# Optimization experiments

Hardware: AMD Instinct MI355X
Metric: run time of the kernel (lower is better)

The kernel has to match this reference:

```python
import jax, jax.numpy as jnp
import numpy as np

GRID_RES = 32      # sparse_grid_dim
GRID_DIM = 8       # dense cells per sparse block side
NUM_EMB = 12000    # number of sparse blocks
EMB_DIM = 1
N_POINTS = 2000000
N_CELLS = GRID_RES * GRID_DIM  # 256^3 virtual dense grid over [-1,1]^3


def _interp_point(pos, embeddings, block_table):
    """Trilinear interp of a sparse block-grid at one world point in [-1,1]^3.

    embeddings: [NUM_EMB, GRID_DIM^3, EMB_DIM]
    block_table: [GRID_RES]^3 int32, block index or -1 if unallocated.
    Returns (emb [EMB_DIM], valid_all bool).
    """
    xc = (pos + 1.0) * 0.5 * (N_CELLS - 1)            # world -> cell coords
    base = jnp.clip(jnp.floor(xc), 0.0, N_CELLS - 2).astype(jnp.int32)
    frac = xc - base.astype(xc.dtype)
    emb = jnp.zeros((EMB_DIM,), xc.dtype)
    valid_all = jnp.bool_(True)
    for dx in (0, 1):
        for dy in (0, 1):
            for dz in (0, 1):
                corner = base + jnp.array([dx, dy, dz], jnp.int32)
                blk = corner // GRID_DIM                 # sparse block coord
                loc = corner % GRID_DIM                  # local cell coord
                bidx = block_table[blk[0], blk[1], blk[2]]
                valid = bidx >= 0
                li = (loc[0] * GRID_DIM + loc[1]) * GRID_DIM + loc[2]
                e = embeddings[jnp.maximum(bidx, 0), li]
                wx = frac[0] if dx else 1.0 - frac[0]
                wy = frac[1] if dy else 1.0 - frac[1]
                wz = frac[2] if dz else 1.0 - frac[2]
                emb = emb + jnp.where(valid, wx * wy * wz, 0.0) * e
                valid_all = jnp.logical_and(valid_all, valid)
    return emb, valid_all


def setup_inputs() -> dict:
    key = jax.random.key(0)
    k1, k2 = jax.random.split(key, 2)
    positions = jax.random.uniform(k1, (N_POINTS, 3), minval=-1.0, maxval=1.0,
                                   dtype=jnp.float32)
    # original init zeros the embeddings; use small randn for a non-trivial test
    embeddings = 0.1 * jax.random.normal(k2, (NUM_EMB, GRID_DIM ** 3, EMB_DIM),
                                         dtype=jnp.float32)
    # sparse occupancy: NUM_EMB random blocks of the GRID_RES^3 lattice allocated
    rng = np.random.default_rng(0)
    table = -np.ones(GRID_RES ** 3, np.int32)
    table[rng.permutation(GRID_RES ** 3)[:NUM_EMB]] = np.arange(NUM_EMB, dtype=np.int32)
    block_table = jnp.asarray(table.reshape(GRID_RES, GRID_RES, GRID_RES))
    return {"positions": positions, "embeddings": embeddings,
            "block_table": block_table}


@jax.jit
def reference(positions, embeddings, block_table):
    def f(pos):
        e, v = _interp_point(pos, embeddings, block_table)
        return e[0], v
    # value_and_grad mirrors torch.autograd.grad(embedding[...,0], positions)
    (emb, mask), grad_x = jax.vmap(jax.value_and_grad(f, has_aux=True))(positions)
    return emb[:, None], grad_x, mask
```

## Files before the change

### kernel.cpp

```cpp
#include <hip/hip_runtime.h>
#include <hip/hip_bf16.h>

#define GRID_RES 32
#define GRID_DIM 8
#define N_CELLS  256
#define EMB_VOL  512
#define NPT      4
#define BLOCK    512
#define TAB_N    (GRID_RES * GRID_RES * GRID_RES)

__global__ __launch_bounds__(BLOCK) void neural_poisson_interp(
    const float* __restrict__ positions,
    const float* __restrict__ embeddings,
    const int*   __restrict__ block_table,
    float* __restrict__ out,
    int n)
{
    __shared__ short stab[TAB_N];

    {
        const int4* t4 = reinterpret_cast<const int4*>(block_table);
        for (int k = threadIdx.x; k < TAB_N / 4; k += BLOCK) {
            int4 v = t4[k];
            short4 s;
            s.x = (short)v.x; s.y = (short)v.y; s.z = (short)v.z; s.w = (short)v.w;
            *reinterpret_cast<short4*>(&stab[4 * k]) = s;
        }
    }
    __syncthreads();

    int t  = blockIdx.x * blockDim.x + threadIdx.x;
    int i0 = t * NPT;
    if (i0 >= n) return;
    bool full = (i0 + NPT <= n);

    float px[NPT], py[NPT], pz[NPT];
    if (full) {
        const float4* p4 = reinterpret_cast<const float4*>(positions + 3 * (size_t)i0);
        float4 A = p4[0], B = p4[1], C = p4[2];
        px[0] = A.x; py[0] = A.y; pz[0] = A.z;
        px[1] = A.w; py[1] = B.x; pz[1] = B.y;
        px[2] = B.z; py[2] = B.w; pz[2] = C.x;
        px[3] = C.y; py[3] = C.z; pz[3] = C.w;
    } else {
#pragma unroll
        for (int p = 0; p < NPT; ++p) {
            int ip = min(i0 + p, n - 1);
            px[p] = positions[3 * ip + 0];
            py[p] = positions[3 * ip + 1];
            pz[p] = positions[3 * ip + 2];
        }
    }

    float wA[NPT][3], wB[NPT][3];
    int   bidx[NPT][8];
    int   li  [NPT][8];

#pragma unroll
    for (int p = 0; p < NPT; ++p) {
        float xc[3];
        xc[0] = (px[p] + 1.0f) * 0.5f * (float)(N_CELLS - 1);
        xc[1] = (py[p] + 1.0f) * 0.5f * (float)(N_CELLS - 1);
        xc[2] = (pz[p] + 1.0f) * 0.5f * (float)(N_CELLS - 1);

        int base[3];
#pragma unroll
        for (int a = 0; a < 3; ++a) {
            float bf = fminf(fmaxf(floorf(xc[a]), 0.0f), (float)(N_CELLS - 2));
            float fr = xc[a] - bf;
            wA[p][a] = 1.0f - fr;
            wB[p][a] = fr;
            base[a] = (int)bf;
        }

#pragma unroll
        for (int c = 0; c < 8; ++c) {
            int dx = (c >> 2) & 1, dy = (c >> 1) & 1, dz = c & 1;
            int cx = base[0] + dx, cy = base[1] + dy, cz = base[2] + dz;
            bidx[p][c] = stab[((cx >> 3) * GRID_RES + (cy >> 3)) * GRID_RES
                              + (cz >> 3)];
            li[p][c] = ((cx & 7) * GRID_DIM + (cy & 7)) * GRID_DIM + (cz & 7);
        }
    }

    float e[NPT][8];
#pragma unroll
    for (int p = 0; p < NPT; ++p)
#pragma unroll
        for (int c = 0; c < 8; ++c) {
            int b = bidx[p][c] > 0 ? bidx[p][c] : 0;
            e[p][c] = embeddings[b * EMB_VOL + li[p][c]];
        }

    const float scale = 0.5f * (float)(N_CELLS - 1);
    float acc[NPT], gxv[NPT], gyv[NPT], gzv[NPT], mk[NPT];

#pragma unroll
    for (int p = 0; p < NPT; ++p) {
        float a = 0.0f, gx = 0.0f, gy = 0.0f, gz = 0.0f;
        bool vall = true;
#pragma unroll
        for (int c = 0; c < 8; ++c) {
            int dx = (c >> 2) & 1, dy = (c >> 1) & 1, dz = c & 1;
            bool valid = bidx[p][c] >= 0;
            vall = vall && valid;
            float ev = valid ? e[p][c] : 0.0f;
            float wx = dx ? wB[p][0] : wA[p][0];
            float wy = dy ? wB[p][1] : wA[p][1];
            float wz = dz ? wB[p][2] : wA[p][2];
            a  += wx * wy * wz * ev;
            float tgx = wy * wz * ev;
            float tgy = wx * wz * ev;
            float tgz = wx * wy * ev;
            gx += dx ? tgx : -tgx;
            gy += dy ? tgy : -tgy;
            gz += dz ? tgz : -tgz;
        }
        acc[p] = a;
        gxv[p] = scale * gx;
        gyv[p] = scale * gy;
        gzv[p] = scale * gz;
        mk[p]  = vall ? 1.0f : 0.0f;
    }

    float* out_emb  = out;
    float* out_grad = out + (size_t)n;
    float* out_mask = out + 4 * (size_t)n;

    if (full) {
        *reinterpret_cast<float4*>(out_emb + i0) =
            make_float4(acc[0], acc[1], acc[2], acc[3]);
        float4* g4 = reinterpret_cast<float4*>(out_grad + 3 * (size_t)i0);
        g4[0] = make_float4(gxv[0], gyv[0], gzv[0], gxv[1]);
        g4[1] = make_float4(gyv[1], gzv[1], gxv[2], gyv[2]);
        g4[2] = make_float4(gzv[2], gxv[3], gyv[3], gzv[3]);
        *reinterpret_cast<float4*>(out_mask + i0) =
            make_float4(mk[0], mk[1], mk[2], mk[3]);
    } else {
#pragma unroll
        for (int p = 0; p < NPT; ++p) {
            int ip = i0 + p;
            if (ip < n) {
                out_emb[ip]          = acc[p];
                out_grad[3 * ip + 0] = gxv[p];
                out_grad[3 * ip + 1] = gyv[p];
                out_grad[3 * ip + 2] = gzv[p];
                out_mask[ip]         = mk[p];
            }
        }
    }
}

extern "C" void kernel_launch(void* const* d_in, const int* in_sizes, int n_in,
                              void* d_out, int out_size, void* d_ws, size_t ws_size,
                              hipStream_t stream) {
    const float* positions   = (const float*)d_in[0];
    const float* embeddings  = (const float*)d_in[1];
    const int*   block_table = (const int*)d_in[2];

    int n = in_sizes[0] / 3;
    int nthreads = (n + NPT - 1) / NPT;

    float* out = (float*)d_out;

    int grid = (nthreads + BLOCK - 1) / BLOCK;
    neural_poisson_interp<<<grid, BLOCK, 0, stream>>>(
        positions, embeddings, block_table, out, n);
}
```

Baseline: 130.2 us.

## Pre-pack z-adjacent embedding pairs as bf16 and use persistent grid

Adds a pre-pass kernel that builds, for each allocated block, a workspace array of packed bf16 pairs (value at z and z+1, including the neighbour block's first z slice). The main kernel then fetches both z corners with one 32-bit load, halving the embedding gathers per point. It also switches to a grid-stride persistent launch capped at 512 blocks, so the shared-memory table load is amortised over many points. The trade-off is bf16 precision loss on embeddings, an extra launch and a pre-pass over all 32768 table entries, and a slow fallback load when only the z+1 block is allocated.

New measurement: 136.8 us. +5.0%, slower.

```diff
diff --git a/kernel.cpp b/kernel.cpp
--- a/kernel.cpp
+++ b/kernel.cpp
@@ -5,19 +5,216 @@
 #define GRID_DIM 8
 #define N_CELLS  256
 #define EMB_VOL  512
+#define TAB_N    (GRID_RES * GRID_RES * GRID_RES)
 #define NPT      4
 #define BLOCK    512
-#define TAB_N    (GRID_RES * GRID_RES * GRID_RES)
+
+
+__device__ __forceinline__ unsigned bf16rne(float f) {
+    unsigned u = __float_as_uint(f);
+    return (u + 0x7fffu + ((u >> 16) & 1u)) >> 16;
+}
+
+__global__ __launch_bounds__(256) void build_pairs(
+    const float* __restrict__ emb, const int* __restrict__ table,
+    unsigned* __restrict__ pb)
+{
+    int tid = blockIdx.x * 256 + threadIdx.x;
+    int entry = tid >> 6;
+    if (entry >= TAB_N) return;
+    int row = tid & 63;
+    int b = table[entry];
+    if (b < 0) return;
+    int BZ = entry & (GRID_RES - 1);
+    int zn = (BZ < GRID_RES - 1) ? table[entry + 1] : -1;
+
+    const float* src = emb + (size_t)b * EMB_VOL + row * 8;
+    float4 a0 = *reinterpret_cast<const float4*>(src);
+    float4 a1 = *reinterpret_cast<const float4*>(src + 4);
+    float e0=a0.x, e1=a0.y, e2=a0.z, e3=a0.w;
+    float e4=a1.x, e5=a1.y, e6=a1.z, e7=a1.w;
+    float e8 = (zn >= 0) ? emb[(size_t)zn * EMB_VOL + row * 8] : 0.0f;
+
+    unsigned o0 = bf16rne(e0) | (bf16rne(e1) << 16);
+    unsigned o1 = bf16rne(e2) | (bf16rne(e3) << 16);
+    unsigned o2 = bf16rne(e4) | (bf16rne(e5) << 16);
+    unsigned o3 = bf16rne(e6) | (bf16rne(e7) << 16);
+    unsigned o4 = bf16rne(e1) | (bf16rne(e2) << 16);
+    unsigned o5 = bf16rne(e3) | (bf16rne(e4) << 16);
+    unsigned o6 = bf16rne(e5) | (bf16rne(e6) << 16);
+    unsigned o7 = bf16rne(e7) | (bf16rne(e8) << 16);
+
+    uint4* dst = reinterpret_cast<uint4*>(pb + (size_t)b * EMB_VOL + row * 8);
+    dst[0] = make_uint4(o0, o1, o2, o3);
+    dst[1] = make_uint4(o4, o5, o6, o7);
+}
+
+__global__ __launch_bounds__(BLOCK) void interp_pairs(
+    const float* __restrict__ positions,
+    const float* __restrict__ emb,
+    const int*   __restrict__ table,
+    const unsigned* __restrict__ pb,
+    float* __restrict__ out, int n)
+{
+    __shared__ short stab[TAB_N];
+    {
+        const int4* t4 = reinterpret_cast<const int4*>(table);
+        for (int k = threadIdx.x; k < TAB_N / 4; k += BLOCK) {
+            int4 v = t4[k];
+            short4 s;
+            s.x = (short)v.x; s.y = (short)v.y; s.z = (short)v.z; s.w = (short)v.w;
+            *reinterpret_cast<short4*>(&stab[4 * k]) = s;
+        }
+    }
+    __syncthreads();
+
+    int nq = (n + NPT - 1) / NPT;
+    int stride = gridDim.x * BLOCK;
+    for (int q = blockIdx.x * BLOCK + threadIdx.x; q < nq; q += stride) {
+        int i0 = q * NPT;
+        bool full = (i0 + NPT <= n);
+
+        float px[NPT], py[NPT], pz[NPT];
+        if (full) {
+            const float4* p4 = reinterpret_cast<const float4*>(positions + 3 * (size_t)i0);
+            float4 A = p4[0], B = p4[1], C = p4[2];
+            px[0]=A.x; py[0]=A.y; pz[0]=A.z;
+            px[1]=A.w; py[1]=B.x; pz[1]=B.y;
+            px[2]=B.z; py[2]=B.w; pz[2]=C.x;
+            px[3]=C.y; py[3]=C.z; pz[3]=C.w;
+        } else {
+#pragma unroll
+            for (int p = 0; p < NPT; ++p) {
+                int ip = min(i0 + p, n - 1);
+                px[p] = positions[3 * ip + 0];
+                py[p] = positions[3 * ip + 1];
+                pz[p] = positions[3 * ip + 2];
+            }
+        }
+
+        float wA[NPT][3], wB[NPT][3];
+        int tb[NPT][4], tb1[NPT][4];
+        unsigned lx4[NPT];
+        int lzv[NPT];
+        unsigned uu[NPT][4];
+
+#pragma unroll
+        for (int p = 0; p < NPT; ++p) {
+            float xc[3];
+            xc[0] = (px[p] + 1.0f) * 0.5f * (float)(N_CELLS - 1);
+            xc[1] = (py[p] + 1.0f) * 0.5f * (float)(N_CELLS - 1);
+            xc[2] = (pz[p] + 1.0f) * 0.5f * (float)(N_CELLS - 1);
+            int base[3];
+#pragma unroll
+            for (int a = 0; a < 3; ++a) {
+                float bf = fminf(fmaxf(floorf(xc[a]), 0.0f), (float)(N_CELLS - 2));
+                float fr = xc[a] - bf;
+                wA[p][a] = 1.0f - fr;
+                wB[p][a] = fr;
+                base[a] = (int)bf;
+            }
+            int bx = base[0], by = base[1], bz = base[2];
+            lzv[p] = bz & 7;
+            int bzs0 = bz >> 3, bzs1 = (bz + 1) >> 3;
+            unsigned pk = 0;
+#pragma unroll
+            for (int c = 0; c < 4; ++c) {
+                int dx = c >> 1, dy = c & 1;
+                int cx = bx + dx, cy = by + dy;
+                int tbase = ((cx >> 3) * GRID_RES + (cy >> 3)) * GRID_RES;
+                tb [p][c] = stab[tbase + bzs0];
+                tb1[p][c] = stab[tbase + bzs1];
+                unsigned lxly = (unsigned)((cx & 7) * 8 + (cy & 7));
+                pk |= lxly << (8 * c);
+            }
+            lx4[p] = pk;
+        }
+
+#pragma unroll
+        for (int p = 0; p < NPT; ++p) {
+            int lz = lzv[p];
+            int zoff = (lz & 1) ? 4 + (lz >> 1) : (lz >> 1);
+#pragma unroll
+            for (int c = 0; c < 4; ++c) {
+                int b = tb[p][c] > 0 ? tb[p][c] : 0;
+                int lxly = (lx4[p] >> (8 * c)) & 0xff;
+                uu[p][c] = pb[(size_t)b * EMB_VOL + lxly * 8 + zoff];
+            }
+        }
+
+        const float scale = 0.5f * (float)(N_CELLS - 1);
+        float acc[NPT], gxv[NPT], gyv[NPT], gzv[NPT], mk[NPT];
+
+#pragma unroll
+        for (int p = 0; p < NPT; ++p) {
+            float wz0 = wA[p][2], wz1 = wB[p][2];
+            float a = 0.0f, gx = 0.0f, gy = 0.0f, gz = 0.0f;
+            bool vall = true;
+#pragma unroll
+            for (int c = 0; c < 4; ++c) {
+                int dx = c >> 1, dy = c & 1;
+                bool v0 = tb [p][c] >= 0;
+                bool v1 = tb1[p][c] >= 0;
+                vall = vall && v0 && v1;
+                unsigned u = uu[p][c];
+                float e0 = v0 ? __uint_as_float(u << 16) : 0.0f;
+                float e1 = v0 ? __uint_as_float(u & 0xffff0000u) : 0.0f;
+                if (!v0 && v1) {
+                    int lxly = (lx4[p] >> (8 * c)) & 0xff;
+                    e1 = emb[(size_t)tb1[p][c] * EMB_VOL + lxly * 8];
+                }
+                float s = wz0 * e0 + wz1 * e1;
+                float wx = dx ? wB[p][0] : wA[p][0];
+                float wy = dy ? wB[p][1] : wA[p][1];
+                float wxy = wx * wy;
+                a  += wxy * s;
+                gx += dx ? wy * s : -wy * s;
+                gy += dy ? wx * s : -wx * s;
+                gz += wxy * (e1 - e0);
+            }
+            acc[p] = a;
+            gxv[p] = scale * gx;
+            gyv[p] = scale * gy;
+            gzv[p] = scale * gz;
+            mk[p]  = vall ? 1.0f : 0.0f;
+        }
+
+        float* out_emb  = out;
+        float* out_grad = out + (size_t)n;
+        float* out_mask = out + 4 * (size_t)n;
+
+        if (full) {
+            *reinterpret_cast<float4*>(out_emb + i0) =
+                make_float4(acc[0], acc[1], acc[2], acc[3]);
+            float4* g4 = reinterpret_cast<float4*>(out_grad + 3 * (size_t)i0);
+            g4[0] = make_float4(gxv[0], gyv[0], gzv[0], gxv[1]);
+            g4[1] = make_float4(gyv[1], gzv[1], gxv[2], gyv[2]);
+            g4[2] = make_float4(gzv[2], gxv[3], gyv[3], gzv[3]);
+            *reinterpret_cast<float4*>(out_mask + i0) =
+                make_float4(mk[0], mk[1], mk[2], mk[3]);
+        } else {
+#pragma unroll
+            for (int p = 0; p < NPT; ++p) {
+                int ip = i0 + p;
+                if (ip < n) {
+                    out_emb[ip]          = acc[p];
+                    out_grad[3 * ip + 0] = gxv[p];
+                    out_grad[3 * ip + 1] = gyv[p];
+                    out_grad[3 * ip + 2] = gzv[p];
+                    out_mask[ip]         = mk[p];
+                }
+            }
+        }
+    }
+}
 
 __global__ __launch_bounds__(BLOCK) void neural_poisson_interp(
     const float* __restrict__ positions,
     const float* __restrict__ embeddings,
     const int*   __restrict__ block_table,
-    float* __restrict__ out,
-    int n)
+    float* __restrict__ out, int n)
 {
     __shared__ short stab[TAB_N];
-
     {
         const int4* t4 = reinterpret_cast<const int4*>(block_table);
         for (int k = threadIdx.x; k < TAB_N / 4; k += BLOCK) {
@@ -29,7 +226,7 @@
     }
     __syncthreads();
 
-    int t  = blockIdx.x * blockDim.x + threadIdx.x;
+    int t = blockIdx.x * blockDim.x + threadIdx.x;
     int i0 = t * NPT;
     if (i0 >= n) return;
     bool full = (i0 + NPT <= n);
@@ -38,10 +235,10 @@
     if (full) {
         const float4* p4 = reinterpret_cast<const float4*>(positions + 3 * (size_t)i0);
         float4 A = p4[0], B = p4[1], C = p4[2];
-        px[0] = A.x; py[0] = A.y; pz[0] = A.z;
-        px[1] = A.w; py[1] = B.x; pz[1] = B.y;
-        px[2] = B.z; py[2] = B.w; pz[2] = C.x;
-        px[3] = C.y; py[3] = C.z; pz[3] = C.w;
+        px[0]=A.x; py[0]=A.y; pz[0]=A.z;
+        px[1]=A.w; py[1]=B.x; pz[1]=B.y;
+        px[2]=B.z; py[2]=B.w; pz[2]=C.x;
+        px[3]=C.y; py[3]=C.z; pz[3]=C.w;
     } else {
 #pragma unroll
         for (int p = 0; p < NPT; ++p) {
@@ -53,36 +250,31 @@
     }
 
     float wA[NPT][3], wB[NPT][3];
-    int   bidx[NPT][8];
-    int   li  [NPT][8];
-
+    int bidx[NPT][8];
+    int li[NPT][8];
 #pragma unroll
     for (int p = 0; p < NPT; ++p) {
         float xc[3];
-        xc[0] = (px[p] + 1.0f) * 0.5f * (float)(N_CELLS - 1);
-        xc[1] = (py[p] + 1.0f) * 0.5f * (float)(N_CELLS - 1);
-        xc[2] = (pz[p] + 1.0f) * 0.5f * (float)(N_CELLS - 1);
-
+        xc[0] = (px[p] + 1.0f) * 0.5f * 255.0f;
+        xc[1] = (py[p] + 1.0f) * 0.5f * 255.0f;
+        xc[2] = (pz[p] + 1.0f) * 0.5f * 255.0f;
         int base[3];
 #pragma unroll
         for (int a = 0; a < 3; ++a) {
-            float bf = fminf(fmaxf(floorf(xc[a]), 0.0f), (float)(N_CELLS - 2));
+            float bf = fminf(fmaxf(floorf(xc[a]), 0.0f), 254.0f);
             float fr = xc[a] - bf;
             wA[p][a] = 1.0f - fr;
             wB[p][a] = fr;
             base[a] = (int)bf;
         }
-
 #pragma unroll
         for (int c = 0; c < 8; ++c) {
             int dx = (c >> 2) & 1, dy = (c >> 1) & 1, dz = c & 1;
             int cx = base[0] + dx, cy = base[1] + dy, cz = base[2] + dz;
-            bidx[p][c] = stab[((cx >> 3) * GRID_RES + (cy >> 3)) * GRID_RES
-                              + (cz >> 3)];
+            bidx[p][c] = stab[((cx >> 3) * GRID_RES + (cy >> 3)) * GRID_RES + (cz >> 3)];
             li[p][c] = ((cx & 7) * GRID_DIM + (cy & 7)) * GRID_DIM + (cz & 7);
         }
     }
-
     float e[NPT][8];
 #pragma unroll
     for (int p = 0; p < NPT; ++p)
@@ -91,10 +283,8 @@
             int b = bidx[p][c] > 0 ? bidx[p][c] : 0;
             e[p][c] = embeddings[b * EMB_VOL + li[p][c]];
         }
-
-    const float scale = 0.5f * (float)(N_CELLS - 1);
+    const float scale = 127.5f;
     float acc[NPT], gxv[NPT], gyv[NPT], gzv[NPT], mk[NPT];
-
 #pragma unroll
     for (int p = 0; p < NPT; ++p) {
         float a = 0.0f, gx = 0.0f, gy = 0.0f, gz = 0.0f;
@@ -108,7 +298,7 @@
             float wx = dx ? wB[p][0] : wA[p][0];
             float wy = dy ? wB[p][1] : wA[p][1];
             float wz = dz ? wB[p][2] : wA[p][2];
-            a  += wx * wy * wz * ev;
+            a += wx * wy * wz * ev;
             float tgx = wy * wz * ev;
             float tgy = wx * wz * ev;
             float tgz = wx * wy * ev;
@@ -116,17 +306,12 @@
             gy += dy ? tgy : -tgy;
             gz += dz ? tgz : -tgz;
         }
-        acc[p] = a;
-        gxv[p] = scale * gx;
-        gyv[p] = scale * gy;
-        gzv[p] = scale * gz;
-        mk[p]  = vall ? 1.0f : 0.0f;
-    }
-
+        acc[p] = a; gxv[p] = scale * gx; gyv[p] = scale * gy; gzv[p] = scale * gz;
+        mk[p] = vall ? 1.0f : 0.0f;
+    }
     float* out_emb  = out;
     float* out_grad = out + (size_t)n;
     float* out_mask = out + 4 * (size_t)n;
-
     if (full) {
         *reinterpret_cast<float4*>(out_emb + i0) =
             make_float4(acc[0], acc[1], acc[2], acc[3]);
@@ -141,11 +326,11 @@
         for (int p = 0; p < NPT; ++p) {
             int ip = i0 + p;
             if (ip < n) {
-                out_emb[ip]          = acc[p];
+                out_emb[ip] = acc[p];
                 out_grad[3 * ip + 0] = gxv[p];
                 out_grad[3 * ip + 1] = gyv[p];
                 out_grad[3 * ip + 2] = gzv[p];
-                out_mask[ip]         = mk[p];
+                out_mask[ip] = mk[p];
             }
         }
     }
@@ -159,11 +344,24 @@
     const int*   block_table = (const int*)d_in[2];
 
     int n = in_sizes[0] / 3;
-    int nthreads = (n + NPT - 1) / NPT;
-
+    int nblocks = in_sizes[1] / EMB_VOL;
+    size_t pair_bytes = (size_t)nblocks * EMB_VOL * sizeof(unsigned);
     float* out = (float*)d_out;
 
-    int grid = (nthreads + BLOCK - 1) / BLOCK;
-    neural_poisson_interp<<<grid, BLOCK, 0, stream>>>(
-        positions, embeddings, block_table, out, n);
-}
+    if (ws_size >= pair_bytes) {
+        unsigned* pb = (unsigned*)d_ws;
+        build_pairs<<<(TAB_N * 64 + 255) / 256, 256, 0, stream>>>(
+            embeddings, block_table, pb);
+        int nq = (n + NPT - 1) / NPT;
+        int grid = 512;
+        int maxg = (nq + BLOCK - 1) / BLOCK;
+        if (grid > maxg) grid = maxg;
+        interp_pairs<<<grid, BLOCK, 0, stream>>>(
+            positions, embeddings, block_table, pb, out, n);
+    } else {
+        int nthreads = (n + NPT - 1) / NPT;
+        int grid = (nthreads + BLOCK - 1) / BLOCK;
+        neural_poisson_interp<<<grid, BLOCK, 0, stream>>>(
+            positions, embeddings, block_table, out, n);
+    }
+}
```

## Use persistent grid-stride blocks to amortize shared block-table load

Applied to the files above, without the earlier changes.

Switches to a fixed grid of 512 blocks of 1024 threads that grid-stride over point pairs, with two points per iteration instead of four. Each block now loads and converts the block table into shared memory once, so the per-block table load is spread over many more points. The narrower per-thread work may lower memory-level parallelism per thread, and the launch-bounds hint may constrain registers.

Result: slower. 176.7 us (+35.7%).

```diff
diff --git a/kernel.cpp b/kernel.cpp
--- a/kernel.cpp
+++ b/kernel.cpp
@@ -5,11 +5,11 @@
 #define GRID_DIM 8
 #define N_CELLS  256
 #define EMB_VOL  512
-#define NPT      4
-#define BLOCK    512
 #define TAB_N    (GRID_RES * GRID_RES * GRID_RES)
+#define NPT      2
+#define BLOCK    1024
 
-__global__ __launch_bounds__(BLOCK) void neural_poisson_interp(
+__global__ __launch_bounds__(BLOCK, 8) void neural_poisson_interp(
     const float* __restrict__ positions,
     const float* __restrict__ embeddings,
     const int*   __restrict__ block_table,
@@ -17,7 +17,6 @@
     int n)
 {
     __shared__ short stab[TAB_N];
-
     {
         const int4* t4 = reinterpret_cast<const int4*>(block_table);
         for (int k = threadIdx.x; k < TAB_N / 4; k += BLOCK) {
@@ -29,123 +28,119 @@
     }
     __syncthreads();
 
-    int t  = blockIdx.x * blockDim.x + threadIdx.x;
-    int i0 = t * NPT;
-    if (i0 >= n) return;
-    bool full = (i0 + NPT <= n);
-
-    float px[NPT], py[NPT], pz[NPT];
-    if (full) {
-        const float4* p4 = reinterpret_cast<const float4*>(positions + 3 * (size_t)i0);
-        float4 A = p4[0], B = p4[1], C = p4[2];
-        px[0] = A.x; py[0] = A.y; pz[0] = A.z;
-        px[1] = A.w; py[1] = B.x; pz[1] = B.y;
-        px[2] = B.z; py[2] = B.w; pz[2] = C.x;
-        px[3] = C.y; py[3] = C.z; pz[3] = C.w;
-    } else {
-#pragma unroll
-        for (int p = 0; p < NPT; ++p) {
-            int ip = min(i0 + p, n - 1);
-            px[p] = positions[3 * ip + 0];
-            py[p] = positions[3 * ip + 1];
-            pz[p] = positions[3 * ip + 2];
-        }
-    }
-
-    float wA[NPT][3], wB[NPT][3];
-    int   bidx[NPT][8];
-    int   li  [NPT][8];
-
-#pragma unroll
-    for (int p = 0; p < NPT; ++p) {
-        float xc[3];
-        xc[0] = (px[p] + 1.0f) * 0.5f * (float)(N_CELLS - 1);
-        xc[1] = (py[p] + 1.0f) * 0.5f * (float)(N_CELLS - 1);
-        xc[2] = (pz[p] + 1.0f) * 0.5f * (float)(N_CELLS - 1);
-
-        int base[3];
-#pragma unroll
-        for (int a = 0; a < 3; ++a) {
-            float bf = fminf(fmaxf(floorf(xc[a]), 0.0f), (float)(N_CELLS - 2));
-            float fr = xc[a] - bf;
-            wA[p][a] = 1.0f - fr;
-            wB[p][a] = fr;
-            base[a] = (int)bf;
-        }
-
-#pragma unroll
-        for (int c = 0; c < 8; ++c) {
-            int dx = (c >> 2) & 1, dy = (c >> 1) & 1, dz = c & 1;
-            int cx = base[0] + dx, cy = base[1] + dy, cz = base[2] + dz;
-            bidx[p][c] = stab[((cx >> 3) * GRID_RES + (cy >> 3)) * GRID_RES
-                              + (cz >> 3)];
-            li[p][c] = ((cx & 7) * GRID_DIM + (cy & 7)) * GRID_DIM + (cz & 7);
-        }
-    }
-
-    float e[NPT][8];
-#pragma unroll
-    for (int p = 0; p < NPT; ++p)
-#pragma unroll
-        for (int c = 0; c < 8; ++c) {
-            int b = bidx[p][c] > 0 ? bidx[p][c] : 0;
-            e[p][c] = embeddings[b * EMB_VOL + li[p][c]];
-        }
-
-    const float scale = 0.5f * (float)(N_CELLS - 1);
-    float acc[NPT], gxv[NPT], gyv[NPT], gzv[NPT], mk[NPT];
-
-#pragma unroll
-    for (int p = 0; p < NPT; ++p) {
-        float a = 0.0f, gx = 0.0f, gy = 0.0f, gz = 0.0f;
-        bool vall = true;
-#pragma unroll
-        for (int c = 0; c < 8; ++c) {
-            int dx = (c >> 2) & 1, dy = (c >> 1) & 1, dz = c & 1;
-            bool valid = bidx[p][c] >= 0;
-            vall = vall && valid;
-            float ev = valid ? e[p][c] : 0.0f;
-            float wx = dx ? wB[p][0] : wA[p][0];
-            float wy = dy ? wB[p][1] : wA[p][1];
-            float wz = dz ? wB[p][2] : wA[p][2];
-            a  += wx * wy * wz * ev;
-            float tgx = wy * wz * ev;
-            float tgy = wx * wz * ev;
-            float tgz = wx * wy * ev;
-            gx += dx ? tgx : -tgx;
-            gy += dy ? tgy : -tgy;
-            gz += dz ? tgz : -tgz;
-        }
-        acc[p] = a;
-        gxv[p] = scale * gx;
-        gyv[p] = scale * gy;
-        gzv[p] = scale * gz;
-        mk[p]  = vall ? 1.0f : 0.0f;
-    }
-
     float* out_emb  = out;
     float* out_grad = out + (size_t)n;
     float* out_mask = out + 4 * (size_t)n;
 
-    if (full) {
-        *reinterpret_cast<float4*>(out_emb + i0) =
-            make_float4(acc[0], acc[1], acc[2], acc[3]);
-        float4* g4 = reinterpret_cast<float4*>(out_grad + 3 * (size_t)i0);
-        g4[0] = make_float4(gxv[0], gyv[0], gzv[0], gxv[1]);
-        g4[1] = make_float4(gyv[1], gzv[1], gxv[2], gyv[2]);
-        g4[2] = make_float4(gzv[2], gxv[3], gyv[3], gzv[3]);
-        *reinterpret_cast<float4*>(out_mask + i0) =
-            make_float4(mk[0], mk[1], mk[2], mk[3]);
-    } else {
+    int nq = (n + NPT - 1) / NPT;
+    int stride = gridDim.x * BLOCK;
+    for (int q = blockIdx.x * BLOCK + threadIdx.x; q < nq; q += stride) {
+        int i0 = q * NPT;
+        bool full = (i0 + NPT <= n);
+
+        float px[NPT], py[NPT], pz[NPT];
+        if (full) {
+            const float2* p2 = reinterpret_cast<const float2*>(positions + 3 * (size_t)i0);
+            float2 A = p2[0], B = p2[1], C = p2[2];
+            px[0] = A.x; py[0] = A.y; pz[0] = B.x;
+            px[1] = B.y; py[1] = C.x; pz[1] = C.y;
+        } else {
+#pragma unroll
+            for (int p = 0; p < NPT; ++p) {
+                int ip = min(i0 + p, n - 1);
+                px[p] = positions[3 * ip + 0];
+                py[p] = positions[3 * ip + 1];
+                pz[p] = positions[3 * ip + 2];
+            }
+        }
+
+        float wA[NPT][3], wB[NPT][3];
+        int bidx[NPT][8];
+        int li  [NPT][8];
+
 #pragma unroll
         for (int p = 0; p < NPT; ++p) {
-            int ip = i0 + p;
-            if (ip < n) {
-                out_emb[ip]          = acc[p];
-                out_grad[3 * ip + 0] = gxv[p];
-                out_grad[3 * ip + 1] = gyv[p];
-                out_grad[3 * ip + 2] = gzv[p];
-                out_mask[ip]         = mk[p];
+            float xc[3];
+            xc[0] = (px[p] + 1.0f) * 0.5f * (float)(N_CELLS - 1);
+            xc[1] = (py[p] + 1.0f) * 0.5f * (float)(N_CELLS - 1);
+            xc[2] = (pz[p] + 1.0f) * 0.5f * (float)(N_CELLS - 1);
+            int base[3];
+#pragma unroll
+            for (int a = 0; a < 3; ++a) {
+                float bf = fminf(fmaxf(floorf(xc[a]), 0.0f), (float)(N_CELLS - 2));
+                float fr = xc[a] - bf;
+                wA[p][a] = 1.0f - fr;
+                wB[p][a] = fr;
+                base[a] = (int)bf;
+            }
+#pragma unroll
+            for (int c = 0; c < 8; ++c) {
+                int dx = (c >> 2) & 1, dy = (c >> 1) & 1, dz = c & 1;
+                int cx = base[0] + dx, cy = base[1] + dy, cz = base[2] + dz;
+                bidx[p][c] = stab[((cx >> 3) * GRID_RES + (cy >> 3)) * GRID_RES
+                                  + (cz >> 3)];
+                li[p][c] = ((cx & 7) * GRID_DIM + (cy & 7)) * GRID_DIM + (cz & 7);
+            }
+        }
+
+        float e[NPT][8];
+#pragma unroll
+        for (int p = 0; p < NPT; ++p)
+#pragma unroll
+            for (int c = 0; c < 8; ++c) {
+                int b = bidx[p][c] > 0 ? bidx[p][c] : 0;
+                e[p][c] = embeddings[b * EMB_VOL + li[p][c]];
+            }
+
+        const float scale = 0.5f * (float)(N_CELLS - 1);
+        float acc[NPT], gxv[NPT], gyv[NPT], gzv[NPT], mk[NPT];
+
+#pragma unroll
+        for (int p = 0; p < NPT; ++p) {
+            float a = 0.0f, gx = 0.0f, gy = 0.0f, gz = 0.0f;
+            bool vall = true;
+#pragma unroll
+            for (int c = 0; c < 8; ++c) {
+                int dx = (c >> 2) & 1, dy = (c >> 1) & 1, dz = c & 1;
+                bool valid = bidx[p][c] >= 0;
+                vall = vall && valid;
+                float ev = valid ? e[p][c] : 0.0f;
+                float wx = dx ? wB[p][0] : wA[p][0];
+                float wy = dy ? wB[p][1] : wA[p][1];
+                float wz = dz ? wB[p][2] : wA[p][2];
+                a += wx * wy * wz * ev;
+                float tgx = wy * wz * ev;
+                float tgy = wx * wz * ev;
+                float tgz = wx * wy * ev;
+                gx += dx ? tgx : -tgx;
+                gy += dy ? tgy : -tgy;
+                gz += dz ? tgz : -tgz;
+            }
+            acc[p] = a;
+            gxv[p] = scale * gx;
+            gyv[p] = scale * gy;
+            gzv[p] = scale * gz;
+            mk[p]  = vall ? 1.0f : 0.0f;
+        }
+
+        if (full) {
+            *reinterpret_cast<float2*>(out_emb + i0)  = make_float2(acc[0], acc[1]);
+            *reinterpret_cast<float2*>(out_mask + i0) = make_float2(mk[0], mk[1]);
+            float2* g2 = reinterpret_cast<float2*>(out_grad + 3 * (size_t)i0);
+            g2[0] = make_float2(gxv[0], gyv[0]);
+            g2[1] = make_float2(gzv[0], gxv[1]);
+            g2[2] = make_float2(gyv[1], gzv[1]);
+        } else {
+#pragma unroll
+            for (int p = 0; p < NPT; ++p) {
+                int ip = i0 + p;
+                if (ip < n) {
+                    out_emb[ip]          = acc[p];
+                    out_grad[3 * ip + 0] = gxv[p];
+                    out_grad[3 * ip + 1] = gyv[p];
+                    out_grad[3 * ip + 2] = gzv[p];
+                    out_mask[ip]         = mk[p];
+                }
             }
         }
     }
@@ -159,11 +154,13 @@
     const int*   block_table = (const int*)d_in[2];
 
     int n = in_sizes[0] / 3;
-    int nthreads = (n + NPT - 1) / NPT;
+    int nq = (n + NPT - 1) / NPT;
 
     float* out = (float*)d_out;
 
-    int grid = (nthreads + BLOCK - 1) / BLOCK;
+    int grid = 512;
+    int maxg = (nq + BLOCK - 1) / BLOCK;
+    if (grid > maxg) grid = maxg;
     neural_poisson_interp<<<grid, BLOCK, 0, stream>>>(
         positions, embeddings, block_table, out, n);
 }
```

## Use grid-stride persistent blocks and paired z-corner float4 embedding loads

Applied to the files above, without the earlier changes.

The launch becomes a grid-stride loop over a fixed grid of 512 blocks. Each block now copies the 64 KB block table into shared memory once and reuses it across many point groups, instead of every short-lived block copying it again. Each pair of z-adjacent corners is fetched with a single float4 load plus an occasional scalar fallback, which cuts gather instructions from 8 to about 4 per point. The interpolation math is refactored to combine z pairs first. The risks are fewer resident waves to hide gather latency and extra select logic for the fallback.

Result: no change. 129.2 us (-0.8%).

```diff
diff --git a/kernel.cpp b/kernel.cpp
--- a/kernel.cpp
+++ b/kernel.cpp
@@ -5,9 +5,9 @@
 #define GRID_DIM 8
 #define N_CELLS  256
 #define EMB_VOL  512
+#define TAB_N    (GRID_RES * GRID_RES * GRID_RES)
 #define NPT      4
 #define BLOCK    512
-#define TAB_N    (GRID_RES * GRID_RES * GRID_RES)
 
 __global__ __launch_bounds__(BLOCK) void neural_poisson_interp(
     const float* __restrict__ positions,
@@ -17,7 +17,6 @@
     int n)
 {
     __shared__ short stab[TAB_N];
-
     {
         const int4* t4 = reinterpret_cast<const int4*>(block_table);
         for (int k = threadIdx.x; k < TAB_N / 4; k += BLOCK) {
@@ -29,123 +28,146 @@
     }
     __syncthreads();
 
-    int t  = blockIdx.x * blockDim.x + threadIdx.x;
-    int i0 = t * NPT;
-    if (i0 >= n) return;
-    bool full = (i0 + NPT <= n);
-
-    float px[NPT], py[NPT], pz[NPT];
-    if (full) {
-        const float4* p4 = reinterpret_cast<const float4*>(positions + 3 * (size_t)i0);
-        float4 A = p4[0], B = p4[1], C = p4[2];
-        px[0] = A.x; py[0] = A.y; pz[0] = A.z;
-        px[1] = A.w; py[1] = B.x; pz[1] = B.y;
-        px[2] = B.z; py[2] = B.w; pz[2] = C.x;
-        px[3] = C.y; py[3] = C.z; pz[3] = C.w;
-    } else {
-#pragma unroll
-        for (int p = 0; p < NPT; ++p) {
-            int ip = min(i0 + p, n - 1);
-            px[p] = positions[3 * ip + 0];
-            py[p] = positions[3 * ip + 1];
-            pz[p] = positions[3 * ip + 2];
-        }
-    }
-
-    float wA[NPT][3], wB[NPT][3];
-    int   bidx[NPT][8];
-    int   li  [NPT][8];
-
-#pragma unroll
-    for (int p = 0; p < NPT; ++p) {
-        float xc[3];
-        xc[0] = (px[p] + 1.0f) * 0.5f * (float)(N_CELLS - 1);
-        xc[1] = (py[p] + 1.0f) * 0.5f * (float)(N_CELLS - 1);
-        xc[2] = (pz[p] + 1.0f) * 0.5f * (float)(N_CELLS - 1);
-
-        int base[3];
-#pragma unroll
-        for (int a = 0; a < 3; ++a) {
-            float bf = fminf(fmaxf(floorf(xc[a]), 0.0f), (float)(N_CELLS - 2));
-            float fr = xc[a] - bf;
-            wA[p][a] = 1.0f - fr;
-            wB[p][a] = fr;
-            base[a] = (int)bf;
-        }
-
-#pragma unroll
-        for (int c = 0; c < 8; ++c) {
-            int dx = (c >> 2) & 1, dy = (c >> 1) & 1, dz = c & 1;
-            int cx = base[0] + dx, cy = base[1] + dy, cz = base[2] + dz;
-            bidx[p][c] = stab[((cx >> 3) * GRID_RES + (cy >> 3)) * GRID_RES
-                              + (cz >> 3)];
-            li[p][c] = ((cx & 7) * GRID_DIM + (cy & 7)) * GRID_DIM + (cz & 7);
-        }
-    }
-
-    float e[NPT][8];
-#pragma unroll
-    for (int p = 0; p < NPT; ++p)
-#pragma unroll
-        for (int c = 0; c < 8; ++c) {
-            int b = bidx[p][c] > 0 ? bidx[p][c] : 0;
-            e[p][c] = embeddings[b * EMB_VOL + li[p][c]];
-        }
-
-    const float scale = 0.5f * (float)(N_CELLS - 1);
-    float acc[NPT], gxv[NPT], gyv[NPT], gzv[NPT], mk[NPT];
-
-#pragma unroll
-    for (int p = 0; p < NPT; ++p) {
-        float a = 0.0f, gx = 0.0f, gy = 0.0f, gz = 0.0f;
-        bool vall = true;
-#pragma unroll
-        for (int c = 0; c < 8; ++c) {
-            int dx = (c >> 2) & 1, dy = (c >> 1) & 1, dz = c & 1;
-            bool valid = bidx[p][c] >= 0;
-            vall = vall && valid;
-            float ev = valid ? e[p][c] : 0.0f;
-            float wx = dx ? wB[p][0] : wA[p][0];
-            float wy = dy ? wB[p][1] : wA[p][1];
-            float wz = dz ? wB[p][2] : wA[p][2];
-            a  += wx * wy * wz * ev;
-            float tgx = wy * wz * ev;
-            float tgy = wx * wz * ev;
-            float tgz = wx * wy * ev;
-            gx += dx ? tgx : -tgx;
-            gy += dy ? tgy : -tgy;
-            gz += dz ? tgz : -tgz;
-        }
-        acc[p] = a;
-        gxv[p] = scale * gx;
-        gyv[p] = scale * gy;
-        gzv[p] = scale * gz;
-        mk[p]  = vall ? 1.0f : 0.0f;
-    }
-
+    const float4* emb4 = reinterpret_cast<const float4*>(embeddings);
     float* out_emb  = out;
     float* out_grad = out + (size_t)n;
     float* out_mask = out + 4 * (size_t)n;
 
-    if (full) {
-        *reinterpret_cast<float4*>(out_emb + i0) =
-            make_float4(acc[0], acc[1], acc[2], acc[3]);
-        float4* g4 = reinterpret_cast<float4*>(out_grad + 3 * (size_t)i0);
-        g4[0] = make_float4(gxv[0], gyv[0], gzv[0], gxv[1]);
-        g4[1] = make_float4(gyv[1], gzv[1], gxv[2], gyv[2]);
-        g4[2] = make_float4(gzv[2], gxv[3], gyv[3], gzv[3]);
-        *reinterpret_cast<float4*>(out_mask + i0) =
-            make_float4(mk[0], mk[1], mk[2], mk[3]);
-    } else {
+    int nq = (n + NPT - 1) / NPT;
+    int stride = gridDim.x * BLOCK;
+    for (int q = blockIdx.x * BLOCK + threadIdx.x; q < nq; q += stride) {
+        int i0 = q * NPT;
+        bool full = (i0 + NPT <= n);
+
+        float px[NPT], py[NPT], pz[NPT];
+        if (full) {
+            const float4* p4 = reinterpret_cast<const float4*>(positions + 3 * (size_t)i0);
+            float4 A = p4[0], B = p4[1], C = p4[2];
+            px[0]=A.x; py[0]=A.y; pz[0]=A.z;
+            px[1]=A.w; py[1]=B.x; pz[1]=B.y;
+            px[2]=B.z; py[2]=B.w; pz[2]=C.x;
+            px[3]=C.y; py[3]=C.z; pz[3]=C.w;
+        } else {
+#pragma unroll
+            for (int p = 0; p < NPT; ++p) {
+                int ip = min(i0 + p, n - 1);
+                px[p] = positions[3 * ip + 0];
+                py[p] = positions[3 * ip + 1];
+                pz[p] = positions[3 * ip + 2];
+            }
+        }
+
+        float wA[NPT][3], wB[NPT][3];
+        int tpk [NPT][4];
+        int off0[NPT][4];
+
 #pragma unroll
         for (int p = 0; p < NPT; ++p) {
-            int ip = i0 + p;
-            if (ip < n) {
-                out_emb[ip]          = acc[p];
-                out_grad[3 * ip + 0] = gxv[p];
-                out_grad[3 * ip + 1] = gyv[p];
-                out_grad[3 * ip + 2] = gzv[p];
-                out_mask[ip]         = mk[p];
+            float xc[3];
+            xc[0] = (px[p] + 1.0f) * 0.5f * (float)(N_CELLS - 1);
+            xc[1] = (py[p] + 1.0f) * 0.5f * (float)(N_CELLS - 1);
+            xc[2] = (pz[p] + 1.0f) * 0.5f * (float)(N_CELLS - 1);
+            int base[3];
+#pragma unroll
+            for (int a = 0; a < 3; ++a) {
+                float bf = fminf(fmaxf(floorf(xc[a]), 0.0f), (float)(N_CELLS - 2));
+                float fr = xc[a] - bf;
+                wA[p][a] = 1.0f - fr;
+                wB[p][a] = fr;
+                base[a] = (int)bf;
+            }
+            int bx = base[0], by = base[1], bz = base[2];
+            int lz = bz & 7;
+            int eidx = ((bx >> 3) * GRID_RES + (by >> 3)) * GRID_RES + (bz >> 3);
+            int ox = ((bx & 7) == 7) ? (GRID_RES * GRID_RES) : 0;
+            int oy = ((by & 7) == 7) ? GRID_RES : 0;
+            int oz = ((bz & 7) == 7) ? 1 : 0;
+#pragma unroll
+            for (int i = 0; i < 4; ++i) {
+                int dx = i >> 1, dy = i & 1;
+                int e0i = eidx + (dx ? ox : 0) + (dy ? oy : 0);
+                int t0 = stab[e0i];
+                int t1 = stab[e0i + oz];
+                tpk[p][i] = (t0 & 0xffff) | (t1 << 16);
+                int row = (((bx + dx) & 7) * 8 + ((by + dy) & 7));
+                off0[p][i] = row * 8 + lz;
+            }
+        }
+
+        float ee0[NPT][4], ee1[NPT][4];
+#pragma unroll
+        for (int p = 0; p < NPT; ++p)
+#pragma unroll
+            for (int i = 0; i < 4; ++i) {
+                int t0 = (short)(tpk[p][i] & 0xffff);
+                int t1 = tpk[p][i] >> 16;
+                int b0 = t0 > 0 ? t0 : 0;
+                int o  = off0[p][i];
+                int sel = o & 3;
+                float4 f = emb4[(size_t)b0 * (EMB_VOL / 4) + (o >> 2)];
+                float e0 = sel == 0 ? f.x : sel == 1 ? f.y : sel == 2 ? f.z : f.w;
+                float e1 = sel == 0 ? f.y : sel == 1 ? f.z : f.w;
+                if (sel == 3) {
+                    int lz7 = (o & 7) == 7;
+                    int bb  = lz7 ? (t1 > 0 ? t1 : 0) : b0;
+                    int oo  = lz7 ? (o & ~7) : (o + 1);
+                    e1 = embeddings[(size_t)bb * EMB_VOL + oo];
+                }
+                ee0[p][i] = t0 >= 0 ? e0 : 0.0f;
+                ee1[p][i] = t1 >= 0 ? e1 : 0.0f;
+            }
+
+        const float scale = 0.5f * (float)(N_CELLS - 1);
+        float acc[NPT], gxv[NPT], gyv[NPT], gzv[NPT], mk[NPT];
+
+#pragma unroll
+        for (int p = 0; p < NPT; ++p) {
+            float wz0 = wA[p][2], wz1 = wB[p][2];
+            float a = 0.0f, gx = 0.0f, gy = 0.0f, gz = 0.0f;
+            int sgn = -1;
+#pragma unroll
+            for (int i = 0; i < 4; ++i) {
+                int t0 = (short)(tpk[p][i] & 0xffff);
+                int t1 = tpk[p][i] >> 16;
+                sgn &= t0 & t1;
+                int dx = i >> 1, dy = i & 1;
+                float e0 = ee0[p][i], e1 = ee1[p][i];
+                float s = wz0 * e0 + wz1 * e1;
+                float wx = dx ? wB[p][0] : wA[p][0];
+                float wy = dy ? wB[p][1] : wA[p][1];
+                float wxy = wx * wy;
+                a  += wxy * s;
+                gx += dx ? wy * s : -wy * s;
+                gy += dy ? wx * s : -wx * s;
+                gz += wxy * (e1 - e0);
+            }
+            acc[p] = a;
+            gxv[p] = scale * gx;
+            gyv[p] = scale * gy;
+            gzv[p] = scale * gz;
+            mk[p]  = (sgn >= 0) ? 1.0f : 0.0f;
+        }
+
+        if (full) {
+            *reinterpret_cast<float4*>(out_emb + i0) =
+                make_float4(acc[0], acc[1], acc[2], acc[3]);
+            float4* g4 = reinterpret_cast<float4*>(out_grad + 3 * (size_t)i0);
+            g4[0] = make_float4(gxv[0], gyv[0], gzv[0], gxv[1]);
+            g4[1] = make_float4(gyv[1], gzv[1], gxv[2], gyv[2]);
+            g4[2] = make_float4(gzv[2], gxv[3], gyv[3], gzv[3]);
+            *reinterpret_cast<float4*>(out_mask + i0) =
+                make_float4(mk[0], mk[1], mk[2], mk[3]);
+        } else {
+#pragma unroll
+            for (int p = 0; p < NPT; ++p) {
+                int ip = i0 + p;
+                if (ip < n) {
+                    out_emb[ip]          = acc[p];
+                    out_grad[3 * ip + 0] = gxv[p];
+                    out_grad[3 * ip + 1] = gyv[p];
+                    out_grad[3 * ip + 2] = gzv[p];
+                    out_mask[ip]         = mk[p];
+                }
             }
         }
     }
@@ -159,11 +181,13 @@
     const int*   block_table = (const int*)d_in[2];
 
     int n = in_sizes[0] / 3;
-    int nthreads = (n + NPT - 1) / NPT;
+    int nq = (n + NPT - 1) / NPT;
 
     float* out = (float*)d_out;
 
-    int grid = (nthreads + BLOCK - 1) / BLOCK;
+    int grid = 512;
+    int maxg = (nq + BLOCK - 1) / BLOCK;
+    if (grid > maxg) grid = maxg;
     neural_poisson_interp<<<grid, BLOCK, 0, stream>>>(
         positions, embeddings, block_table, out, n);
 }
```
